# Optimization experiments

Hardware: AMD Instinct MI355X
Metric: run time of the kernel (lower is better)

Reference implementation:

```python
import jax, jax.numpy as jnp
import numpy as np

B, N, M, F_DIM, H, D = 4, 2048, 2048, 512, 8, 64  # M == num_time
MID = H * D
EPS = 1e-5


def _layernorm(x, w, b):
    mu = jnp.mean(x, axis=-1, keepdims=True)
    var = jnp.var(x, axis=-1, keepdims=True)
    return (x - mu) * jax.lax.rsqrt(var + EPS) * w + b


def setup_inputs() -> dict:
    key = jax.random.key(0)
    ks = jax.random.split(key, 12)
    s = 0.02
    return {
        "x": jax.random.normal(ks[0], (B, N, F_DIM), jnp.float32),
        "context": jax.random.normal(ks[1], (B, M, F_DIM), jnp.float32),
        "pos_emb": jax.random.normal(ks[2], (M, F_DIM), jnp.float32) * s,  # nn.Embedding(num_time, features)
        "ln_w": jnp.ones((F_DIM,), jnp.float32),
        "ln_b": jnp.zeros((F_DIM,), jnp.float32),
        "lnc_w": jnp.ones((F_DIM,), jnp.float32),
        "lnc_b": jnp.zeros((F_DIM,), jnp.float32),
        "Wq": jax.random.normal(ks[3], (F_DIM, MID), jnp.float32) * s,
        "Wk": jax.random.normal(ks[4], (F_DIM, MID), jnp.float32) * s,
        "Wv": jax.random.normal(ks[5], (F_DIM, MID), jnp.float32) * s,
        "Wout": jax.random.normal(ks[6], (MID, F_DIM), jnp.float32) * s,
        "bout": jnp.zeros((F_DIM,), jnp.float32),
    }


def reference(x, context, pos_emb, ln_w, ln_b, lnc_w, lnc_b, Wq, Wk, Wv, Wout, bout):
    scale = D ** (-0.5)
    keys = jnp.broadcast_to(pos_emb[None], (x.shape[0], M, F_DIM))  # [B, T, F]
    xn = _layernorm(x, ln_w, ln_b)
    kn = _layernorm(keys, ln_w, ln_b)          # same norm as x (self.norm)
    cn = _layernorm(context, lnc_w, lnc_b)
    q = (xn @ Wq).reshape(x.shape[0], N, H, D).transpose(0, 2, 1, 3)  # b h n d
    k = (kn @ Wk).reshape(x.shape[0], M, H, D).transpose(0, 2, 1, 3)  # b h m d
    v = (cn @ Wv).reshape(x.shape[0], M, H, D).transpose(0, 2, 1, 3)  # b h m d
    sim = jnp.einsum('bhnd,bhmd->bhnm', q, k) * scale
    attn = jax.nn.softmax(sim, axis=-1)
    out = jnp.einsum('bhnm,bhmd->bhnd', attn, v)
    out = out.transpose(0, 2, 1, 3).reshape(x.shape[0], N, MID)  # b n (h d)
    return out @ Wout + bout
```

## Files before the change

kernel.cpp:

```cpp
#include <hip/hip_runtime.h>
#include <stdint.h>

#define B_ 4
#define N_ 2048
#define M_ 2048
#define F_ 512
#define H_ 8
#define D_ 64

typedef __bf16 bf16x8 __attribute__((ext_vector_type(8)));
typedef float f32x4 __attribute__((ext_vector_type(4)));
typedef float f32x16 __attribute__((ext_vector_type(16)));

typedef const __attribute__((address_space(1))) uint32_t* gas_ptr;
typedef __attribute__((address_space(3))) uint32_t* las_ptr;

__device__ inline ushort f32_bf16(float f) {
    union { float f; uint32_t u; } v; v.f = f;
    uint32_t r = v.u + 0x7FFFu + ((v.u >> 16) & 1u);
    return (ushort)(r >> 16);
}

__global__ __launch_bounds__(128) void prep_kernel(
    const float* __restrict__ x, const float* __restrict__ ctx, const float* __restrict__ pos,
    const float* __restrict__ lnw, const float* __restrict__ lnb,
    const float* __restrict__ lncw, const float* __restrict__ lncb,
    const float* __restrict__ Wq, const float* __restrict__ Wk,
    const float* __restrict__ Wv, const float* __restrict__ Wo,
    ushort* __restrict__ xn, ushort* __restrict__ kn, ushort* __restrict__ cn,
    ushort* __restrict__ WqT, ushort* __restrict__ WkT,
    ushort* __restrict__ WvT, ushort* __restrict__ WoT)
{
    __shared__ float red[4];
    __shared__ float tile[32][33];
    int r = blockIdx.x;
    int tid = threadIdx.x;

    if (r < B_ * N_ + M_ + B_ * M_) {
        const float* src; ushort* dst; const float* w; const float* bp;
        if (r < B_ * N_) {
            src = x + (size_t)r * F_; dst = xn + (size_t)r * F_; w = lnw; bp = lnb;
        } else if (r < B_ * N_ + M_) {
            int rr = r - B_ * N_;
            src = pos + (size_t)rr * F_; dst = kn + (size_t)rr * F_; w = lnw; bp = lnb;
        } else {
            int rr = r - (B_ * N_ + M_);
            src = ctx + (size_t)rr * F_; dst = cn + (size_t)rr * F_; w = lncw; bp = lncb;
        }
        int wave = tid >> 6, lane = tid & 63;
        float4 v = reinterpret_cast<const float4*>(src)[tid];
        float s = v.x + v.y + v.z + v.w;
        float sq = v.x * v.x + v.y * v.y + v.z * v.z + v.w * v.w;
        #pragma unroll
        for (int mask = 1; mask < 64; mask <<= 1) {
            s += __shfl_xor(s, mask, 64);
            sq += __shfl_xor(sq, mask, 64);
        }
        if (lane == 0) { red[wave * 2] = s; red[wave * 2 + 1] = sq; }
        __syncthreads();
        float S = red[0] + red[2], SQ = red[1] + red[3];
        float mean = S * (1.0f / F_);
        float var = SQ * (1.0f / F_) - mean * mean;
        float rstd = rsqrtf(var + 1e-5f);
        float4 wv = reinterpret_cast<const float4*>(w)[tid];
        float4 bv = reinterpret_cast<const float4*>(bp)[tid];
        ushort4 o;
        o.x = f32_bf16((v.x - mean) * rstd * wv.x + bv.x);
        o.y = f32_bf16((v.y - mean) * rstd * wv.y + bv.y);
        o.z = f32_bf16((v.z - mean) * rstd * wv.z + bv.z);
        o.w = f32_bf16((v.w - mean) * rstd * wv.w + bv.w);
        reinterpret_cast<ushort4*>(dst)[tid] = o;
        return;
    }

    int wblk = r - (B_ * N_ + M_ + B_ * M_);
    const float* W; ushort* WT;
    switch (wblk >> 8) {
        case 0: W = Wq; WT = WqT; break;
        case 1: W = Wk; WT = WkT; break;
        case 2: W = Wv; WT = WvT; break;
        default: W = Wo; WT = WoT; break;
    }
    int ti = wblk & 255;
    int n0 = (ti & 15) * 32, k0 = (ti >> 4) * 32;
    int tx = tid & 31, ty = tid >> 5;
    #pragma unroll
    for (int j = 0; j < 8; ++j)
        tile[ty + j * 4][tx] = W[(size_t)(k0 + ty + j * 4) * F_ + n0 + tx];
    __syncthreads();
    #pragma unroll
    for (int j = 0; j < 8; ++j)
        WT[(size_t)(n0 + ty + j * 4) * F_ + k0 + tx] = f32_bf16(tile[tx][ty + j * 4]);
}

__device__ __forceinline__ void gemm_body(
    const ushort* __restrict__ A, const ushort* __restrict__ BT,
    const float* __restrict__ bias, void* __restrict__ Cout,
    int mode, int bx, int by)
{
    __shared__ ushort As[128][64];
    __shared__ ushort Bs[128][64];
    int tid = threadIdx.x;
    int row0 = by * 128, col0 = bx * 128;
    int wv = tid >> 6, lane = tid & 63;
    int wm = wv >> 1, wn = wv & 1;
    f32x4 acc[4][4] = {};

    const int lrow8 = lane >> 3;
    const int chs = ((lane & 7) ^ (lrow8 & 7)) * 8;
    const ushort* agp = A + (size_t)(row0 + wv * 32 + lrow8) * F_ + chs;
    const ushort* bgp = BT + (size_t)(col0 + wv * 32 + lrow8) * F_ + chs;

    for (int k0 = 0; k0 < F_; k0 += 64) {
        #pragma unroll
        for (int j = 0; j < 4; ++j) {
            __builtin_amdgcn_global_load_lds(
                (gas_ptr)(const void*)(agp + k0 + j * 8 * F_),
                (las_ptr)(void*)&As[wv * 32 + j * 8][0], 16, 0, 0);
            __builtin_amdgcn_global_load_lds(
                (gas_ptr)(const void*)(bgp + k0 + j * 8 * F_),
                (las_ptr)(void*)&Bs[wv * 32 + j * 8][0], 16, 0, 0);
        }
        __syncthreads();
        #pragma unroll
        for (int kt = 0; kt < 2; ++kt) {
            int lrow = lane & 15;
            int ch = ((kt * 4 + (lane >> 4)) ^ (lane & 7)) * 8;
            bf16x8 af[4], bfr[4];
            #pragma unroll
            for (int mt = 0; mt < 4; ++mt)
                af[mt] = *reinterpret_cast<const bf16x8*>(&As[wm * 64 + mt * 16 + lrow][ch]);
            #pragma unroll
            for (int nt = 0; nt < 4; ++nt)
                bfr[nt] = *reinterpret_cast<const bf16x8*>(&Bs[wn * 64 + nt * 16 + lrow][ch]);
            #pragma unroll
            for (int mt = 0; mt < 4; ++mt)
                #pragma unroll
                for (int nt = 0; nt < 4; ++nt)
                    acc[mt][nt] = __builtin_amdgcn_mfma_f32_16x16x32_bf16(
                        af[mt], bfr[nt], acc[mt][nt], 0, 0, 0);
        }
        __syncthreads();
    }

    int lr4 = (lane >> 4) * 4, lc = lane & 15;
    #pragma unroll
    for (int mt = 0; mt < 4; ++mt) {
        #pragma unroll
        for (int nt = 0; nt < 4; ++nt) {
            int ccol = col0 + wn * 64 + nt * 16 + lc;
            float bv = (mode == 1) ? bias[ccol] : 0.0f;
            #pragma unroll
            for (int j = 0; j < 4; ++j) {
                int crow = row0 + wm * 64 + mt * 16 + lr4 + j;
                float val = acc[mt][nt][j] + bv;
                if (mode == 1) {
                    reinterpret_cast<float*>(Cout)[(size_t)crow * F_ + ccol] = val;
                } else if (mode == 0) {
                    reinterpret_cast<ushort*>(Cout)[(size_t)crow * F_ + ccol] =
                        f32_bf16(val * 0.18033688f);
                } else if (mode == 2) {
                    int h = ccol >> 6, t = crow >> 7, s = (crow >> 6) & 1;
                    int ab = (crow >> 5) & 1, l31 = crow & 31;
                    int ds = (ccol >> 4) & 3, g2 = (ccol >> 3) & 1, e = ccol & 7;
                    size_t addr = (((size_t)(h * 16 + t) * 16 + s * 8 + ds * 2 + ab) * 64
                                   + g2 * 32 + l31) * 8 + e;
                    reinterpret_cast<ushort*>(Cout)[addr] = f32_bf16(val);
                } else {
                    int b2 = crow >> 11, m = crow & 2047;
                    int h = ccol >> 6, d = ccol & 63;
                    int bh = b2 * 8 + h, hh = d >> 5, l31 = d & 31;
                    int t = m >> 7, s = (m >> 6) & 1, s_ = (m >> 4) & 3;
                    int g2 = (m >> 3) & 1, i = m & 7;
                    size_t addr = (((size_t)(bh * 16 + t) * 16 + hh * 8 + s * 4 + s_) * 64
                                   + g2 * 32 + l31) * 8 + i;
                    reinterpret_cast<ushort*>(Cout)[addr] = f32_bf16(val);
                }
            }
        }
    }
}

__global__ __launch_bounds__(256) void qkv_gemm_kernel(
    const ushort* __restrict__ xn, const ushort* __restrict__ kn,
    const ushort* __restrict__ cn,
    const ushort* __restrict__ WqT, const ushort* __restrict__ WkT,
    const ushort* __restrict__ WvT,
    ushort* __restrict__ qb, ushort* __restrict__ kF, ushort* __restrict__ vF)
{
    int bid = blockIdx.x;
    if (bid < 256) {
        gemm_body(xn, WqT, nullptr, (void*)qb, 0, bid & 3, bid >> 2);
    } else if (bid < 320) {
        int t = bid - 256;
        gemm_body(kn, WkT, nullptr, (void*)kF, 2, t & 3, t >> 2);
    } else {
        int t = bid - 320;
        gemm_body(cn, WvT, nullptr, (void*)vF, 3, t & 3, t >> 2);
    }
}

__global__ __launch_bounds__(256) void out_gemm_kernel(
    const ushort* __restrict__ A, const ushort* __restrict__ WoT,
    const float* __restrict__ bias, float* __restrict__ out)
{
    gemm_body(A, WoT, bias, (void*)out, 1, blockIdx.x & 3, blockIdx.x >> 2);
}

#define MAKE_PA(dst, p, ss) do {                                               \
    uint32_t w0_, w1_, w2_, w3_;                                               \
    asm("v_cvt_pk_bf16_f32 %0, %1, %2" : "=v"(w0_) : "v"(p[8*(ss)+0]), "v"(p[8*(ss)+1])); \
    asm("v_cvt_pk_bf16_f32 %0, %1, %2" : "=v"(w1_) : "v"(p[8*(ss)+2]), "v"(p[8*(ss)+3])); \
    asm("v_cvt_pk_bf16_f32 %0, %1, %2" : "=v"(w2_) : "v"(p[8*(ss)+4]), "v"(p[8*(ss)+5])); \
    asm("v_cvt_pk_bf16_f32 %0, %1, %2" : "=v"(w3_) : "v"(p[8*(ss)+6]), "v"(p[8*(ss)+7])); \
    asm("v_permlane32_swap_b32 %0, %1" : "+v"(w0_), "+v"(w2_));                \
    asm("v_permlane32_swap_b32 %0, %1" : "+v"(w1_), "+v"(w3_));                \
    union { uint32_t w[4]; bf16x8 v; } u_;                                     \
    u_.w[0] = w0_; u_.w[1] = w1_; u_.w[2] = w2_; u_.w[3] = w3_;                \
    dst = u_.v;                                                                \
} while (0)

#define KLOAD(DST, u) do {                                                     \
    const ushort* _p = kfb_ + (size_t)(u) * 4096 + lane * 8;                   \
    _Pragma("unroll")                                                          \
    for (int f_ = 0; f_ < 8; ++f_)                                             \
        DST[f_] = *reinterpret_cast<const bf16x8*>(_p + f_ * 512);             \
} while (0)

#define VLOAD(DST, u) do {                                                     \
    const ushort* _p = vfb_ + (size_t)((u) >> 1) * 8192 +                      \
                       ((u) & 1) * 4 * 512 + lane * 8;                         \
    _Pragma("unroll")                                                          \
    for (int hh_ = 0; hh_ < 2; ++hh_)                                          \
        _Pragma("unroll")                                                      \
        for (int s2_ = 0; s2_ < 4; ++s2_)                                      \
            DST[hh_ * 4 + s2_] = *reinterpret_cast<const bf16x8*>(             \
                _p + (hh_ * 8 + s2_) * 512);                                   \
} while (0)

#define COMPUTE_HALF(QF, OACC, LR, AB) do {                                    \
    f32x16 sS;                                                                 \
    _Pragma("unroll")                                                          \
    for (int j = 0; j < 16; ++j) sS[j] = 0.0f;                                 \
    __builtin_amdgcn_s_setprio(1);                                             \
    _Pragma("unroll")                                                          \
    for (int ds_ = 0; ds_ < 4; ++ds_)                                          \
        sS = __builtin_amdgcn_mfma_f32_32x32x16_bf16(kR[ds_ * 2 + (AB)], QF[ds_], sS, 0, 0, 0); \
    __builtin_amdgcn_s_setprio(0);                                             \
    float pf[16];                                                              \
    _Pragma("unroll")                                                          \
    for (int j = 0; j < 16; ++j)                                               \
        pf[j] = __builtin_amdgcn_exp2f(sS[j]);                                 \
    float r0 = 0.0f, r1 = 0.0f, r2 = 0.0f, r3 = 0.0f;                          \
    _Pragma("unroll")                                                          \
    for (int j = 0; j < 16; j += 4) {                                          \
        r0 += pf[j];     r1 += pf[j + 1];                                      \
        r2 += pf[j + 2]; r3 += pf[j + 3];                                      \
    }                                                                          \
    LR += (r0 + r1) + (r2 + r3);                                               \
    bf16x8 pa0, pa1;                                                           \
    MAKE_PA(pa0, pf, 0);                                                       \
    MAKE_PA(pa1, pf, 1);                                                       \
    __builtin_amdgcn_s_setprio(1);                                             \
    _Pragma("unroll")                                                          \
    for (int hh = 0; hh < 2; ++hh) {                                           \
        OACC[hh] = __builtin_amdgcn_mfma_f32_32x32x16_bf16(                    \
            pa0, vR[hh * 4 + (AB) * 2], OACC[hh], 0, 0, 0);                    \
        OACC[hh] = __builtin_amdgcn_mfma_f32_32x32x16_bf16(                    \
            pa1, vR[hh * 4 + (AB) * 2 + 1], OACC[hh], 0, 0, 0);                \
    }                                                                          \
    __builtin_amdgcn_s_setprio(0);                                             \
} while (0)

__global__ __launch_bounds__(512, 1) void attn_kernel(
    const ushort* __restrict__ q,
    const ushort* __restrict__ kF,
    const ushort* __restrict__ vF,
    ushort* __restrict__ o)
{
    const int wave = threadIdx.x >> 6, lane = threadIdx.x & 63;
    const int l31 = lane & 31, g = lane >> 5;
    const int qpair = wave & 3, half = wave >> 2;
    const int bid = blockIdx.x;
    const int qx = bid >> 5, bh = bid & 31;
    const int b = bh >> 3, h = bh & 7;
    const int q0 = qx * 256 + qpair * 64;

    __shared__ float ols[4][64][64];
    __shared__ float lls[4][2][64];

    bf16x8 qfA[4], qfB[4];
    const ushort* qrowA = q + (size_t)(b * N_ + q0 + l31) * F_ + h * 64 + g * 8;
    const ushort* qrowB = qrowA + 32 * F_;
    #pragma unroll
    for (int ds = 0; ds < 4; ++ds) {
        qfA[ds] = *reinterpret_cast<const bf16x8*>(qrowA + ds * 16);
        qfB[ds] = *reinterpret_cast<const bf16x8*>(qrowB + ds * 16);
    }

    float l0 = 0.0f, l1 = 0.0f;
    f32x16 oaccA[2], oaccB[2];
    #pragma unroll
    for (int hh = 0; hh < 2; ++hh)
        #pragma unroll
        for (int j = 0; j < 16; ++j) { oaccA[hh][j] = 0.0f; oaccB[hh][j] = 0.0f; }

    const ushort* kfb_ = kF + (size_t)h * 16 * 16 * 512;
    const ushort* vfb_ = vF + (size_t)bh * 16 * 16 * 512;

    bf16x8 kR[8], vR[8];
    const int ubase = half * 16;

    #pragma unroll 1
    for (int uu = 0; uu < 16; ++uu) {
        int u = ubase + uu;
        KLOAD(kR, u);
        VLOAD(vR, u);
        COMPUTE_HALF(qfA, oaccA, l0, 0);
        COMPUTE_HALF(qfB, oaccB, l1, 0);
        COMPUTE_HALF(qfA, oaccA, l0, 1);
        COMPUTE_HALF(qfB, oaccB, l1, 1);
    }

    l0 += __shfl_xor(l0, 32, 64);
    l1 += __shfl_xor(l1, 32, 64);

    if (half) {
        #pragma unroll
        for (int hh = 0; hh < 2; ++hh)
            #pragma unroll
            for (int j = 0; j < 16; ++j) {
                ols[qpair][hh * 16 + j][lane] = oaccA[hh][j];
                ols[qpair][32 + hh * 16 + j][lane] = oaccB[hh][j];
            }
        lls[qpair][0][lane] = l0;
        lls[qpair][1][lane] = l1;
    }
    __syncthreads();
    if (!half) {
        #pragma unroll
        for (int hh = 0; hh < 2; ++hh)
            #pragma unroll
            for (int j = 0; j < 16; ++j) {
                oaccA[hh][j] += ols[qpair][hh * 16 + j][lane];
                oaccB[hh][j] += ols[qpair][32 + hh * 16 + j][lane];
            }
        l0 += lls[qpair][0][lane];
        l1 += lls[qpair][1][lane];
        float li0 = 1.0f / l0, li1 = 1.0f / l1;
        float rli0[16], rli1[16];
        #pragma unroll
        for (int j = 0; j < 16; ++j) {
            int idx = 8 * (j >> 2) + 4 * g + (j & 3);
            rli0[j] = __shfl(li0, idx, 64);
            rli1[j] = __shfl(li1, idx, 64);
        }
        #pragma unroll
        for (int hh = 0; hh < 2; ++hh)
            #pragma unroll
            for (int j = 0; j < 16; ++j) {
                int qr = (j & 3) + 8 * (j >> 2) + 4 * g;
                o[(size_t)(b * N_ + q0 + qr) * F_ + h * 64 + hh * 32 + l31] =
                    f32_bf16(oaccA[hh][j] * rli0[j]);
                o[(size_t)(b * N_ + q0 + 32 + qr) * F_ + h * 64 + hh * 32 + l31] =
                    f32_bf16(oaccB[hh][j] * rli1[j]);
            }
    }
}

extern "C" void kernel_launch(void* const* d_in, const int* in_sizes, int n_in,
                              void* d_out, int out_size, void* d_ws, size_t ws_size,
                              hipStream_t stream) {
    const float* x    = (const float*)d_in[0];
    const float* ctx  = (const float*)d_in[1];
    const float* pos  = (const float*)d_in[2];
    const float* lnw  = (const float*)d_in[3];
    const float* lnb  = (const float*)d_in[4];
    const float* lncw = (const float*)d_in[5];
    const float* lncb = (const float*)d_in[6];
    const float* Wq   = (const float*)d_in[7];
    const float* Wk   = (const float*)d_in[8];
    const float* Wv   = (const float*)d_in[9];
    const float* Wo   = (const float*)d_in[10];
    const float* bout = (const float*)d_in[11];
    float* out = (float*)d_out;

    char* ws = (char*)d_ws;
    ushort* xn  = (ushort*)(ws + 0);
    ushort* cn  = (ushort*)(ws + 8388608);
    ushort* kn  = (ushort*)(ws + 16777216);
    ushort* WqT = (ushort*)(ws + 18874368);
    ushort* WkT = (ushort*)(ws + 19398656);
    ushort* WvT = (ushort*)(ws + 19922944);
    ushort* WoT = (ushort*)(ws + 20447232);
    ushort* qb  = (ushort*)(ws + 20971520);
    ushort* kFb = (ushort*)(ws + 29360128);
    ushort* vFb = (ushort*)(ws + 39845888);
    ushort* ao  = (ushort*)(ws + 48234496);

    hipLaunchKernelGGL(prep_kernel, dim3(B_ * N_ + M_ + B_ * M_ + 1024), dim3(128),
                       0, stream,
                       x, ctx, pos, lnw, lnb, lncw, lncb, Wq, Wk, Wv, Wo,
                       xn, kn, cn, WqT, WkT, WvT, WoT);
    hipLaunchKernelGGL(qkv_gemm_kernel, dim3(576), dim3(256), 0, stream,
                       xn, kn, cn, WqT, WkT, WvT, qb, kFb, vFb);
    hipLaunchKernelGGL(attn_kernel, dim3(256), dim3(512), 0, stream,
                       qb, kFb, vFb, ao);
    hipLaunchKernelGGL(out_gemm_kernel, dim3(256), dim3(256), 0, stream,
                       ao, WoT, bout, out);
}
```

Baseline: 89.95 us.

## Double-buffer LDS tiles in projection GEMM to overlap loads with MFMA

The projection GEMM now uses two LDS buffers per operand and issues the async global-to-LDS loads for the next K slice before computing on the current one, with a single barrier per iteration. This is meant to hide global load latency behind the MFMA work instead of stalling on each tile. It doubles LDS use per block (to 64 KB), which may lower occupancy. Correctness depends on the barrier at the end of each iteration also covering completion of the async loads.

```diff
diff --git a/kernel.cpp b/kernel.cpp
--- a/kernel.cpp
+++ b/kernel.cpp
@@ -93,13 +93,25 @@
         WT[(size_t)(n0 + ty + j * 4) * F_ + k0 + tx] = f32_bf16(tile[tx][ty + j * 4]);
 }
 
+#define GSTAGE(BSEL, KOFS) do {                                                \
+    _Pragma("unroll")                                                          \
+    for (int j_ = 0; j_ < 4; ++j_) {                                           \
+        __builtin_amdgcn_global_load_lds(                                      \
+            (gas_ptr)(const void*)(agp + (KOFS) + j_ * 8 * F_),                \
+            (las_ptr)(void*)&As[BSEL][wv * 32 + j_ * 8][0], 16, 0, 0);         \
+        __builtin_amdgcn_global_load_lds(                                      \
+            (gas_ptr)(const void*)(bgp + (KOFS) + j_ * 8 * F_),                \
+            (las_ptr)(void*)&Bs[BSEL][wv * 32 + j_ * 8][0], 16, 0, 0);         \
+    }                                                                          \
+} while (0)
+
 __device__ __forceinline__ void gemm_body(
     const ushort* __restrict__ A, const ushort* __restrict__ BT,
     const float* __restrict__ bias, void* __restrict__ Cout,
     int mode, int bx, int by)
 {
-    __shared__ ushort As[128][64];
-    __shared__ ushort Bs[128][64];
+    __shared__ ushort As[2][128][64];
+    __shared__ ushort Bs[2][128][64];
     int tid = threadIdx.x;
     int row0 = by * 128, col0 = bx * 128;
     int wv = tid >> 6, lane = tid & 63;
@@ -111,17 +123,12 @@
     const ushort* agp = A + (size_t)(row0 + wv * 32 + lrow8) * F_ + chs;
     const ushort* bgp = BT + (size_t)(col0 + wv * 32 + lrow8) * F_ + chs;
 
-    for (int k0 = 0; k0 < F_; k0 += 64) {
-        #pragma unroll
-        for (int j = 0; j < 4; ++j) {
-            __builtin_amdgcn_global_load_lds(
-                (gas_ptr)(const void*)(agp + k0 + j * 8 * F_),
-                (las_ptr)(void*)&As[wv * 32 + j * 8][0], 16, 0, 0);
-            __builtin_amdgcn_global_load_lds(
-                (gas_ptr)(const void*)(bgp + k0 + j * 8 * F_),
-                (las_ptr)(void*)&Bs[wv * 32 + j * 8][0], 16, 0, 0);
-        }
-        __syncthreads();
+    GSTAGE(0, 0);
+    __syncthreads();
+    int cur = 0;
+    #pragma unroll 1
+    for (int t = 0; t < 8; ++t) {
+        if (t < 7) GSTAGE(cur ^ 1, (t + 1) * 64);
         #pragma unroll
         for (int kt = 0; kt < 2; ++kt) {
             int lrow = lane & 15;
@@ -129,10 +136,10 @@
             bf16x8 af[4], bfr[4];
             #pragma unroll
             for (int mt = 0; mt < 4; ++mt)
-                af[mt] = *reinterpret_cast<const bf16x8*>(&As[wm * 64 + mt * 16 + lrow][ch]);
+                af[mt] = *reinterpret_cast<const bf16x8*>(&As[cur][wm * 64 + mt * 16 + lrow][ch]);
             #pragma unroll
             for (int nt = 0; nt < 4; ++nt)
-                bfr[nt] = *reinterpret_cast<const bf16x8*>(&Bs[wn * 64 + nt * 16 + lrow][ch]);
+                bfr[nt] = *reinterpret_cast<const bf16x8*>(&Bs[cur][wn * 64 + nt * 16 + lrow][ch]);
             #pragma unroll
             for (int mt = 0; mt < 4; ++mt)
                 #pragma unroll
@@ -141,6 +148,7 @@
                         af[mt], bfr[nt], acc[mt][nt], 0, 0, 0);
         }
         __syncthreads();
+        cur ^= 1;
     }
 
     int lr4 = (lane >> 4) * 4, lc = lane & 15;
```

After: 95.12 us. 5.7% more time.
